# Kernel tuning notes

Measured on AMD Instinct MI355X. Metric: run time of the kernel, lower is better.

The kernel has to match this reference:

```python
import jax, jax.numpy as jnp
import numpy as np

N = 16384
S = 7
B = 2
C = 20
LAMBD_COORD = 5.0
LAMBD_NOOBJ = 0.5
EPS = 1e-6


def _rel2abs(box):
    """Convert (xcr_rcell, ycr_rcell, wr, hr, ...) cell-relative boxes on an
    (N,S,S,>=4) grid to absolute corner boxes (xmin,ymin,xmax,ymax) in [0,1]."""
    col = jnp.arange(S, dtype=box.dtype)[None, None, :]  # x cell index j
    row = jnp.arange(S, dtype=box.dtype)[None, :, None]  # y cell index i
    xc = (box[..., 0] + col) / S
    yc = (box[..., 1] + row) / S
    w = box[..., 2]
    h = box[..., 3]
    half_w = w * 0.5
    half_h = h * 0.5
    return jnp.stack([xc - half_w, yc - half_h, xc + half_w, yc + half_h], axis=-1)


def _iou(b1, b2):
    """Elementwise IoU of corner boxes (..., 4)."""
    xi1 = jnp.maximum(b1[..., 0], b2[..., 0])
    yi1 = jnp.maximum(b1[..., 1], b2[..., 1])
    xi2 = jnp.minimum(b1[..., 2], b2[..., 2])
    yi2 = jnp.minimum(b1[..., 3], b2[..., 3])
    inter = jnp.clip(xi2 - xi1, 0.0) * jnp.clip(yi2 - yi1, 0.0)
    a1 = (b1[..., 2] - b1[..., 0]) * (b1[..., 3] - b1[..., 1])
    a2 = (b2[..., 2] - b2[..., 0]) * (b2[..., 3] - b2[..., 1])
    return inter / (a1 + a2 - inter + EPS)


def setup_inputs() -> dict:
    key = jax.random.key(0)
    k1, k2, k3, k4 = jax.random.split(key, 4)
    prediction = jax.random.uniform(k1, (N, S, S, B * 5 + C), dtype=jnp.float32)
    conf = (jax.random.uniform(k2, (N, S, S)) > 0.7).astype(jnp.float32)[..., None]
    boxes = jax.random.uniform(k3, (N, S, S, 4), dtype=jnp.float32) * conf
    cls = jax.nn.one_hot(jax.random.randint(k4, (N, S, S), 0, C), C, dtype=jnp.float32) * conf
    target = jnp.concatenate([boxes, conf, cls], axis=-1)  # (N,S,S,5+C)
    return {"prediction": prediction, "target": target}


def reference(prediction, target):
    n = prediction.shape[0]

    # Absolute boxes; target box zeroed where no object (mul by confidence).
    tgt_abs = _rel2abs(target[..., :5]) * target[..., 4:5]
    pred_abs1 = _rel2abs(prediction[..., :5])
    pred_abs2 = _rel2abs(prediction[..., 5:10])

    iou1 = _iou(tgt_abs, pred_abs1)  # (N,S,S)
    iou2 = _iou(tgt_abs, pred_abs2)

    # Faithful to torch: idx = (iou1 > iou2)*5, i.e. gather box2 when iou1 > iou2.
    pick_box2 = (iou1 > iou2)[..., None]
    xywhc_hat = jnp.where(pick_box2, prediction[..., 5:10], prediction[..., :5])

    xy_hat = xywhc_hat[..., :2]
    wh_hat = xywhc_hat[..., 2:4]
    c_hat = xywhc_hat[..., 4:5]

    xy = target[..., :2]
    wh = target[..., 2:4]
    conf = target[..., 4:5]
    noobj = conf == 0.0  # identity_obj in torch code

    def sse(t, p):
        return jnp.sum((t - p) ** 2)

    # _coordloss: clamp(min=0), zero where noobj, sum-MSE / N
    loss_xy = sse(xy, jnp.where(noobj, 0.0, jnp.clip(xy_hat, 0.0))) / n
    # _sizeloss: clamp(min=0), zero where noobj, sqrt(sum + eps) / N
    loss_wh = jnp.sqrt(sse(wh, jnp.where(noobj, 0.0, jnp.clip(wh_hat, 0.0))) + EPS) / n
    # _confidenceloss: clamp to [0,1], mask, sum-MSE / N (obj and noobj variants)
    c_hat_clamped = jnp.clip(c_hat, 0.0, 1.0)
    loss_conf_obj = sse(conf, jnp.where(noobj, 0.0, c_hat_clamped)) / n
    loss_conf_noobj = sse(conf, jnp.where(~noobj, 0.0, c_hat_clamped)) / n
    # _classloss: no clamp, zero where noobj
    loss_class = sse(target[..., 5:], jnp.where(noobj, 0.0, prediction[..., 10:])) / n

    loss = (LAMBD_COORD * loss_xy + LAMBD_COORD * loss_wh + loss_conf_obj
            + LAMBD_NOOBJ * loss_conf_noobj + loss_class)
    return (loss_xy, loss_wh, loss_conf_obj, loss_conf_noobj, loss_class, loss)
```

## Files before the change

kernel.cpp:

```cpp
#include <hip/hip_runtime.h>
#include <math.h>

constexpr int TOT    = 16384 * 7 * 7;
constexpr int TILE   = 64;
constexpr int NTILES = TOT / TILE;
constexpr int NBLK   = 1280;
constexpr float INV_N = 1.0f / 16384.0f;
constexpr float INV7  = 1.0f / 7.0f;

constexpr int PRED_TILE_B = TILE * 30 * 4;
constexpr int TGT_TILE_B  = TILE * 25 * 4;
constexpr int BUF_B       = 14336;

__device__ __forceinline__ float fast_rcp(float x) {
    return __builtin_amdgcn_rcpf(x);
}

__device__ __forceinline__ void dma16(const void* g, void* lds) {
    __builtin_amdgcn_global_load_lds(
        (const __attribute__((address_space(1))) void*)g,
        (__attribute__((address_space(3))) void*)lds, 16, 0, 0);
}

__global__ __launch_bounds__(64) void yolo_partial(
    const float* __restrict__ pred, const float* __restrict__ tgt,
    float* __restrict__ part )
{
    __shared__ float4 smem4[2 * BUF_B / 16];
    char* smem = (char*)smem4;

    const int l   = threadIdx.x;
    const int bid = blockIdx.x;

    float a_xy = 0.0f, a_wh = 0.0f, a_co = 0.0f, a_cn = 0.0f, a_cl = 0.0f;

    const int nt = (NTILES - bid + NBLK - 1) / NBLK;

    float4 tr0, tr1, tr2, tr3, tr4, tr5, tr6;

#define LD_TGT(tile_)                                                       \
    {                                                                       \
        const float4* gt4 = reinterpret_cast<const float4*>(               \
            tgt + (long)(tile_) * (TILE * 25));                             \
        tr0 = gt4[l];        tr1 = gt4[l + 64];  tr2 = gt4[l + 128];        \
        tr3 = gt4[l + 192];  tr4 = gt4[l + 256]; tr5 = gt4[l + 320];        \
        if (l < 16) tr6 = gt4[l + 384];                                     \
    }

#define DMA_PRED(tile_, b)                                                  \
    {                                                                       \
        const char* gp = (const char*)pred + (long)(tile_) * PRED_TILE_B;   \
        char* lb = smem + (b) * BUF_B;                                      \
        _Pragma("unroll")                                                   \
        for (int i = 0; i < 7; ++i)                                         \
            dma16(gp + (size_t)(l + i * 64) * 16, lb + i * 1024);           \
        if (l < 32) dma16(gp + (size_t)(l + 448) * 16, lb + 7168);          \
    }

#define ST_TGT(b)                                                           \
    {                                                                       \
        float4* st4 = reinterpret_cast<float4*>(smem + (b) * BUF_B + 7680); \
        st4[l]       = tr0;  st4[l + 64]  = tr1;  st4[l + 128] = tr2;       \
        st4[l + 192] = tr3;  st4[l + 256] = tr4;  st4[l + 320] = tr5;       \
        if (l < 16) st4[l + 384] = tr6;                                     \
    }

    LD_TGT(bid);
    DMA_PRED(bid, 0);
    asm volatile("s_waitcnt vmcnt(8)" ::: "memory");
    __builtin_amdgcn_sched_barrier(0);
    ST_TGT(0);
    int buf = 0;

    for (int k = 0; k < nt; ++k) {
        const int tile = bid + k * NBLK;
        if (k + 1 < nt) {
            LD_TGT(bid + (k + 1) * NBLK);
            DMA_PRED(bid + (k + 1) * NBLK, buf ^ 1);
            asm volatile("s_waitcnt vmcnt(15)" ::: "memory");
        } else {
            asm volatile("s_waitcnt vmcnt(0)" ::: "memory");
        }
        __builtin_amdgcn_sched_barrier(0);

        const float* pred_s = (const float*)(smem + buf * BUF_B);
        const float* tgt_s  = pred_s + TILE * 30;

        const int   cell = tile * TILE + l;
        const int   col  = cell % 7;
        const int   row  = (cell / 7) % 7;
        const float fcol = (float)col, frow = (float)row;

        float pv[30];
        {
            const float2* p2 = reinterpret_cast<const float2*>(pred_s + l * 30);
#pragma unroll
            for (int i = 0; i < 15; ++i) {
                float2 v = p2[i];
                pv[2 * i] = v.x; pv[2 * i + 1] = v.y;
            }
        }
        float tv[25];
        {
            const float* tp = tgt_s + l * 25;
#pragma unroll
            for (int kk = 0; kk < 25; ++kk) tv[kk] = tp[kk];
        }

        const float conf  = tv[4];
        const bool  noobj = (conf == 0.0f);

        float xc = (tv[0] + fcol) * INV7, yc = (tv[1] + frow) * INV7;
        float hw = tv[2] * 0.5f,          hh = tv[3] * 0.5f;
        float tx1 = (xc - hw) * conf, ty1 = (yc - hh) * conf;
        float tx2 = (xc + hw) * conf, ty2 = (yc + hh) * conf;
        float t_area = (tx2 - tx1) * (ty2 - ty1);

        float xc1 = (pv[0] + fcol) * INV7, yc1 = (pv[1] + frow) * INV7;
        float hw1 = pv[2] * 0.5f,          hh1 = pv[3] * 0.5f;
        float bx1 = xc1 - hw1, by1 = yc1 - hh1, bx2 = xc1 + hw1, by2 = yc1 + hh1;
        float xi1 = fmaxf(tx1, bx1), yi1 = fmaxf(ty1, by1);
        float xi2 = fminf(tx2, bx2), yi2 = fminf(ty2, by2);
        float inter1 = fmaxf(xi2 - xi1, 0.0f) * fmaxf(yi2 - yi1, 0.0f);
        float area1  = (bx2 - bx1) * (by2 - by1);
        float iou1 = inter1 * fast_rcp(t_area + area1 - inter1 + 1e-6f);

        float xc2 = (pv[5] + fcol) * INV7, yc2 = (pv[6] + frow) * INV7;
        float hw2 = pv[7] * 0.5f,          hh2 = pv[8] * 0.5f;
        float cx1 = xc2 - hw2, cy1 = yc2 - hh2, cx2 = xc2 + hw2, cy2 = yc2 + hh2;
        float xj1 = fmaxf(tx1, cx1), yj1 = fmaxf(ty1, cy1);
        float xj2 = fminf(tx2, cx2), yj2 = fminf(ty2, cy2);
        float inter2 = fmaxf(xj2 - xj1, 0.0f) * fmaxf(yj2 - yj1, 0.0f);
        float area2  = (cx2 - cx1) * (cy2 - cy1);
        float iou2 = inter2 * fast_rcp(t_area + area2 - inter2 + 1e-6f);

        const bool pick2 = iou1 > iou2;
        float hx  = pick2 ? pv[5] : pv[0];
        float hy  = pick2 ? pv[6] : pv[1];
        float hwv = pick2 ? pv[7] : pv[2];
        float hhv = pick2 ? pv[8] : pv[3];
        float hc  = pick2 ? pv[9] : pv[4];

        float px = noobj ? 0.0f : fmaxf(hx, 0.0f);
        float py = noobj ? 0.0f : fmaxf(hy, 0.0f);
        float dx = tv[0] - px, dy = tv[1] - py;
        a_xy += dx * dx + dy * dy;
        float pw = noobj ? 0.0f : fmaxf(hwv, 0.0f);
        float ph = noobj ? 0.0f : fmaxf(hhv, 0.0f);
        float dw = tv[2] - pw, dh = tv[3] - ph;
        a_wh += dw * dw + dh * dh;
        float cc = fminf(fmaxf(hc, 0.0f), 1.0f);
        float co = noobj ? 0.0f : cc;
        float cn = noobj ? cc : 0.0f;
        float dco = conf - co, dcn = conf - cn;
        a_co += dco * dco;
        a_cn += dcn * dcn;
        float clv = 0.0f;
#pragma unroll
        for (int kk = 0; kk < 20; ++kk) {
            float pc = noobj ? 0.0f : pv[10 + kk];
            float d  = tv[5 + kk] - pc;
            clv += d * d;
        }
        a_cl += clv;

        if (k + 1 < nt) {
            asm volatile("s_waitcnt vmcnt(8)" ::: "memory");
            __builtin_amdgcn_sched_barrier(0);
            ST_TGT(buf ^ 1);
            __builtin_amdgcn_sched_barrier(0);
        }
        buf ^= 1;
    }

#pragma unroll
    for (int off = 32; off > 0; off >>= 1) {
        a_xy += __shfl_down(a_xy, off);
        a_wh += __shfl_down(a_wh, off);
        a_co += __shfl_down(a_co, off);
        a_cn += __shfl_down(a_cn, off);
        a_cl += __shfl_down(a_cl, off);
    }
    if (l == 0) {
        float4* r = reinterpret_cast<float4*>(part + bid * 8);
        r[0] = make_float4(a_xy, a_wh, a_co, a_cn);
        r[1] = make_float4(a_cl, 0.0f, 0.0f, 0.0f);
    }
#undef LD_TGT
#undef DMA_PRED
#undef ST_TGT
}

__global__ __launch_bounds__(256) void yolo_final(
    const float* __restrict__ part, float* __restrict__ out)
{
    const int t = threadIdx.x;
    float s0 = 0.0f, s1 = 0.0f, s2 = 0.0f, s3 = 0.0f, s4 = 0.0f;
#pragma unroll
    for (int i = 0; i < NBLK / 256; ++i) {
        const float4* r = reinterpret_cast<const float4*>(part + (t + i * 256) * 8);
        float4 v0 = r[0], v1 = r[1];
        s0 += v0.x; s1 += v0.y; s2 += v0.z; s3 += v0.w; s4 += v1.x;
    }
#pragma unroll
    for (int off = 32; off > 0; off >>= 1) {
        s0 += __shfl_down(s0, off);
        s1 += __shfl_down(s1, off);
        s2 += __shfl_down(s2, off);
        s3 += __shfl_down(s3, off);
        s4 += __shfl_down(s4, off);
    }
    __shared__ float red[4][5];
    const int lane = t & 63, wid = t >> 6;
    if (lane == 0) {
        red[wid][0] = s0; red[wid][1] = s1; red[wid][2] = s2;
        red[wid][3] = s3; red[wid][4] = s4;
    }
    __syncthreads();
    if (t == 0) {
        float r0 = red[0][0] + red[1][0] + red[2][0] + red[3][0];
        float r1 = red[0][1] + red[1][1] + red[2][1] + red[3][1];
        float r2 = red[0][2] + red[1][2] + red[2][2] + red[3][2];
        float r3 = red[0][3] + red[1][3] + red[2][3] + red[3][3];
        float r4 = red[0][4] + red[1][4] + red[2][4] + red[3][4];
        float lxy = r0 * INV_N;
        float lwh = sqrtf(r1 + 1e-6f) * INV_N;
        float lco = r2 * INV_N;
        float lcn = r3 * INV_N;
        float lcl = r4 * INV_N;
        out[0] = lxy;
        out[1] = lwh;
        out[2] = lco;
        out[3] = lcn;
        out[4] = lcl;
        out[5] = 5.0f * lxy + 5.0f * lwh + lco + 0.5f * lcn + lcl;
    }
}

extern "C" void kernel_launch(void* const* d_in, const int* in_sizes, int n_in,
                              void* d_out, int out_size, void* d_ws, size_t ws_size,
                              hipStream_t stream)
{
    const float* pred = (const float*)d_in[0];
    const float* tgt  = (const float*)d_in[1];
    float* out  = (float*)d_out;
    float* part = (float*)d_ws;

    yolo_partial<<<NBLK, 64, 0, stream>>>(pred, tgt, part);
    yolo_final<<<1, 256, 0, stream>>>(part, out);
}
```

Before: 34.02 us.

## Fuse final reduction into main kernel via slotted atomics and last-block ticket

```diff
diff --git a/kernel.cpp b/kernel.cpp
--- a/kernel.cpp
+++ b/kernel.cpp
@@ -5,6 +5,8 @@
 constexpr int TILE   = 64;
 constexpr int NTILES = TOT / TILE;
 constexpr int NBLK   = 1280;
+constexpr int NSLOT  = 16;
+constexpr int SLOT_STRIDE = 32;
 constexpr float INV_N = 1.0f / 16384.0f;
 constexpr float INV7  = 1.0f / 7.0f;
 
@@ -24,7 +26,8 @@
 
 __global__ __launch_bounds__(64) void yolo_partial(
     const float* __restrict__ pred, const float* __restrict__ tgt,
-    float* __restrict__ part )
+    float* __restrict__ acc ,
+    float* __restrict__ out)
 {
     __shared__ float4 smem4[2 * BUF_B / 16];
     char* smem = (char*)smem4;
@@ -181,60 +184,57 @@
         a_cn += __shfl_down(a_cn, off);
         a_cl += __shfl_down(a_cl, off);
     }
+
+    unsigned* ticket = reinterpret_cast<unsigned*>(acc + NSLOT * SLOT_STRIDE);
+    int last = 0;
     if (l == 0) {
-        float4* r = reinterpret_cast<float4*>(part + bid * 8);
-        r[0] = make_float4(a_xy, a_wh, a_co, a_cn);
-        r[1] = make_float4(a_cl, 0.0f, 0.0f, 0.0f);
+        float* slot = acc + (bid & (NSLOT - 1)) * SLOT_STRIDE;
+        atomicAdd(&slot[0], a_xy);
+        atomicAdd(&slot[1], a_wh);
+        atomicAdd(&slot[2], a_co);
+        atomicAdd(&slot[3], a_cn);
+        atomicAdd(&slot[4], a_cl);
+        unsigned t = __hip_atomic_fetch_add(ticket, 1u, __ATOMIC_ACQ_REL,
+                                            __HIP_MEMORY_SCOPE_AGENT);
+        last = (t == (unsigned)(NBLK - 1));
+    }
+    last = __shfl(last, 0);
+
+    if (last) {
+        float s0 = 0.0f, s1 = 0.0f, s2 = 0.0f, s3 = 0.0f, s4 = 0.0f;
+        if (l < NSLOT) {
+            const float* slot = acc + l * SLOT_STRIDE;
+            s0 = __hip_atomic_load(&slot[0], __ATOMIC_RELAXED, __HIP_MEMORY_SCOPE_AGENT);
+            s1 = __hip_atomic_load(&slot[1], __ATOMIC_RELAXED, __HIP_MEMORY_SCOPE_AGENT);
+            s2 = __hip_atomic_load(&slot[2], __ATOMIC_RELAXED, __HIP_MEMORY_SCOPE_AGENT);
+            s3 = __hip_atomic_load(&slot[3], __ATOMIC_RELAXED, __HIP_MEMORY_SCOPE_AGENT);
+            s4 = __hip_atomic_load(&slot[4], __ATOMIC_RELAXED, __HIP_MEMORY_SCOPE_AGENT);
+        }
+#pragma unroll
+        for (int off = 8; off > 0; off >>= 1) {
+            s0 += __shfl_down(s0, off);
+            s1 += __shfl_down(s1, off);
+            s2 += __shfl_down(s2, off);
+            s3 += __shfl_down(s3, off);
+            s4 += __shfl_down(s4, off);
+        }
+        if (l == 0) {
+            float lxy = s0 * INV_N;
+            float lwh = sqrtf(s1 + 1e-6f) * INV_N;
+            float lco = s2 * INV_N;
+            float lcn = s3 * INV_N;
+            float lcl = s4 * INV_N;
+            out[0] = lxy;
+            out[1] = lwh;
+            out[2] = lco;
+            out[3] = lcn;
+            out[4] = lcl;
+            out[5] = 5.0f * lxy + 5.0f * lwh + lco + 0.5f * lcn + lcl;
+        }
     }
 #undef LD_TGT
 #undef DMA_PRED
 #undef ST_TGT
-}
-
-__global__ __launch_bounds__(256) void yolo_final(
-    const float* __restrict__ part, float* __restrict__ out)
-{
-    const int t = threadIdx.x;
-    float s0 = 0.0f, s1 = 0.0f, s2 = 0.0f, s3 = 0.0f, s4 = 0.0f;
-#pragma unroll
-    for (int i = 0; i < NBLK / 256; ++i) {
-        const float4* r = reinterpret_cast<const float4*>(part + (t + i * 256) * 8);
-        float4 v0 = r[0], v1 = r[1];
-        s0 += v0.x; s1 += v0.y; s2 += v0.z; s3 += v0.w; s4 += v1.x;
-    }
-#pragma unroll
-    for (int off = 32; off > 0; off >>= 1) {
-        s0 += __shfl_down(s0, off);
-        s1 += __shfl_down(s1, off);
-        s2 += __shfl_down(s2, off);
-        s3 += __shfl_down(s3, off);
-        s4 += __shfl_down(s4, off);
-    }
-    __shared__ float red[4][5];
-    const int lane = t & 63, wid = t >> 6;
-    if (lane == 0) {
-        red[wid][0] = s0; red[wid][1] = s1; red[wid][2] = s2;
-        red[wid][3] = s3; red[wid][4] = s4;
-    }
-    __syncthreads();
-    if (t == 0) {
-        float r0 = red[0][0] + red[1][0] + red[2][0] + red[3][0];
-        float r1 = red[0][1] + red[1][1] + red[2][1] + red[3][1];
-        float r2 = red[0][2] + red[1][2] + red[2][2] + red[3][2];
-        float r3 = red[0][3] + red[1][3] + red[2][3] + red[3][3];
-        float r4 = red[0][4] + red[1][4] + red[2][4] + red[3][4];
-        float lxy = r0 * INV_N;
-        float lwh = sqrtf(r1 + 1e-6f) * INV_N;
-        float lco = r2 * INV_N;
-        float lcn = r3 * INV_N;
-        float lcl = r4 * INV_N;
-        out[0] = lxy;
-        out[1] = lwh;
-        out[2] = lco;
-        out[3] = lcn;
-        out[4] = lcl;
-        out[5] = 5.0f * lxy + 5.0f * lwh + lco + 0.5f * lcn + lcl;
-    }
 }
 
 extern "C" void kernel_launch(void* const* d_in, const int* in_sizes, int n_in,
@@ -243,9 +243,10 @@
 {
     const float* pred = (const float*)d_in[0];
     const float* tgt  = (const float*)d_in[1];
-    float* out  = (float*)d_out;
-    float* part = (float*)d_ws;
-
-    yolo_partial<<<NBLK, 64, 0, stream>>>(pred, tgt, part);
-    yolo_final<<<1, 256, 0, stream>>>(part, out);
-}
+    float* out = (float*)d_out;
+    float* acc = (float*)d_ws;
+
+    hipMemsetAsync(acc, 0, (NSLOT * SLOT_STRIDE) * sizeof(float) + sizeof(unsigned),
+                   stream);
+    yolo_partial<<<NBLK, 64, 0, stream>>>(pred, tgt, acc, out);
+}
```

Result: slower. 63.78 us (+87.5%).
